# Performance work log

Measured on AMD Instinct MI355X. Metric: run time of the kernel, lower is better.

Reference implementation:

```python
import jax, jax.numpy as jnp
import numpy as np

N, E, F, C, K, H = 100000, 1600000, 64, 32, 8, 36


def setup_inputs() -> dict:
    key = jax.random.key(0)
    ks = jax.random.split(key, 24)
    s = 0.1
    inp = {
        "x": jax.random.normal(ks[0], (N, F), jnp.float32),
        "edge_index": jax.random.randint(ks[1], (2, E), 0, N, dtype=jnp.int32),
        # ChebConv conv1_1: K x [F, H] weights + bias
        "W1_1": jax.random.normal(ks[2], (K, F, H), jnp.float32) * s,
        "b1_1": jnp.zeros((H,), jnp.float32),
        "g1_1": jnp.ones((H,), jnp.float32),
        "be1_1": jnp.zeros((H,), jnp.float32),
        # ChebConv conv1_2: K x [H, H]
        "W1_2": jax.random.normal(ks[3], (K, H, H), jnp.float32) * s,
        "b1_2": jnp.zeros((H,), jnp.float32),
        "g1_2": jnp.ones((H,), jnp.float32),
        "be1_2": jnp.zeros((H,), jnp.float32),
        # GINConv MLP: Linear(F,H) -> ReLU -> Linear(H,H)
        "gin_w1": jax.random.normal(ks[4], (F, H), jnp.float32) * s,
        "gin_b1": jnp.zeros((H,), jnp.float32),
        "gin_w2": jax.random.normal(ks[5], (H, H), jnp.float32) * s,
        "gin_b2": jnp.zeros((H,), jnp.float32),
        "g2": jnp.ones((H,), jnp.float32),
        "be2": jnp.zeros((H,), jnp.float32),
        # conv4: ChebConv K=1 on concat(3H) -> C  (pure linear, no propagation)
        "W4": jax.random.normal(ks[6], (1, 3 * H, C), jnp.float32) * s,
        "b4": jnp.zeros((C,), jnp.float32),
    }
    return inp


def _spmm(w, src, dst, x, n):
    # out[i] = sum_{e: dst_e=i} w_e * x[src_e]
    return jax.ops.segment_sum(w[:, None] * x[src], dst, num_segments=n)


def _cheb(x, src, dst, w, Wk, b):
    # PyG ChebConv with sym norm, lambda_max=2: L_hat = -D^-1/2 A D^-1/2 (loop weight 0)
    n = x.shape[0]
    Kk = Wk.shape[0]
    Tx0 = x
    out = Tx0 @ Wk[0]
    if Kk > 1:
        Tx1 = _spmm(w, src, dst, Tx0, n)
        out = out + Tx1 @ Wk[1]
        for k in range(2, Kk):
            Tx2 = 2.0 * _spmm(w, src, dst, Tx1, n) - Tx0
            out = out + Tx2 @ Wk[k]
            Tx0, Tx1 = Tx1, Tx2
    return out + b


def _bn(x, g, b, eps=1e-5):
    m = jnp.mean(x, axis=0)
    v = jnp.mean(jnp.square(x - m), axis=0)  # biased var, training-mode BN
    return g * (x - m) * jax.lax.rsqrt(v + eps) + b


def reference(x, edge_index, W1_1, b1_1, g1_1, be1_1, W1_2, b1_2, g1_2, be1_2,
              gin_w1, gin_b1, gin_w2, gin_b2, g2, be2, W4, b4):
    src, dst = edge_index[0], edge_index[1]
    n = x.shape[0]
    deg = jax.ops.segment_sum(jnp.ones((src.shape[0],), x.dtype), src, num_segments=n)
    dis = jnp.where(deg > 0, jax.lax.rsqrt(jnp.maximum(deg, 1.0)), 0.0)
    w = -dis[src] * dis[dst]  # scaled Laplacian edge weights

    x1_1 = jax.nn.relu(_bn(_cheb(x, src, dst, w, W1_1, b1_1), g1_1, be1_1))
    x1_2 = jax.nn.relu(_bn(_cheb(x1_1, src, dst, w, W1_2, b1_2), g1_2, be1_2))

    # GINConv (eps=0): nn(x + sum_{j in N(i)} x_j)
    agg = jax.ops.segment_sum(x[src], dst, num_segments=n)
    h = x + agg
    gin = jax.nn.relu(h @ gin_w1 + gin_b1) @ gin_w2 + gin_b2
    x2 = _bn(jax.nn.relu(gin), g2, be2)

    x4 = jnp.concatenate((x1_1, x1_2, x2), axis=1)
    return x4 @ W4[0] + b4
```

## Files before the change

### kernel.cpp

```cpp
#include <hip/hip_runtime.h>

constexpr int N_NODES = 100000;
constexpr int N_EDGES = 1600000;
constexpr int NBK  = 391;
constexpr int NBLK = 640;
constexpr int CHUNK = 2500;
constexpr int LCNT = NBK * NBLK;
constexpr int SCAN_BLKS = (LCNT + 255) / 256;


__device__ __forceinline__ unsigned bf16pack(float a, float b) {
    unsigned ua = __float_as_uint(a), ub = __float_as_uint(b);
    ua += 0x7fffu + ((ua >> 16) & 1u);
    ub += 0x7fffu + ((ub >> 16) & 1u);
    return (ua >> 16) | (ub & 0xffff0000u);
}
__device__ __forceinline__ float bflo(unsigned p) { return __uint_as_float(p << 16); }
__device__ __forceinline__ float bfhi(unsigned p) { return __uint_as_float(p & 0xffff0000u); }


__global__ __launch_bounds__(256) void part_count_kernel(
    const int* __restrict__ ei, int* __restrict__ cntD, int* __restrict__ cntS) {
    __shared__ int hd[NBK], hs[NBK];
    int tid = threadIdx.x;
    for (int i = tid; i < NBK; i += 256) { hd[i] = 0; hs[i] = 0; }
    __syncthreads();
    int e0 = blockIdx.x * CHUNK;
    for (int e = e0 + tid; e < e0 + CHUNK; e += 256) {
        int s = ei[e], d = ei[N_EDGES + e];
        atomicAdd(&hs[s >> 8], 1);
        atomicAdd(&hd[d >> 8], 1);
    }
    __syncthreads();
    for (int i = tid; i < NBK; i += 256) {
        cntD[i * NBLK + blockIdx.x] = hd[i];
        cntS[i * NBLK + blockIdx.x] = hs[i];
    }
}

__global__ __launch_bounds__(256) void scanA_kernel(const int* __restrict__ in,
                                                    int* __restrict__ out,
                                                    int* __restrict__ bsum, int L) {
    __shared__ int sm[256];
    int i = blockIdx.x * 256 + threadIdx.x;
    int v = (i < L) ? in[i] : 0;
    sm[threadIdx.x] = v;
    __syncthreads();
    for (int off = 1; off < 256; off <<= 1) {
        int t = (threadIdx.x >= off) ? sm[threadIdx.x - off] : 0;
        __syncthreads();
        sm[threadIdx.x] += t;
        __syncthreads();
    }
    if (i < L) out[i] = sm[threadIdx.x] - v;
    if (threadIdx.x == 255) bsum[blockIdx.x] = sm[255];
}

__global__ __launch_bounds__(1024) void scanB_kernel(int* __restrict__ bsum, int nb) {
    __shared__ int sm[1024];
    int t = threadIdx.x;
    int v = (t < nb) ? bsum[t] : 0;
    sm[t] = v;
    __syncthreads();
    for (int off = 1; off < 1024; off <<= 1) {
        int u = (t >= off) ? sm[t - off] : 0;
        __syncthreads();
        sm[t] += u;
        __syncthreads();
    }
    if (t < nb) bsum[t] = sm[t] - v;
}

__global__ __launch_bounds__(256) void scanC_kernel(int* __restrict__ out,
                                                    const int* __restrict__ bsum, int L) {
    int i = blockIdx.x * 256 + threadIdx.x;
    if (i < L) out[i] += bsum[blockIdx.x];
}

__global__ __launch_bounds__(256) void part_scatter_kernel(
    const int* __restrict__ ei, const int* __restrict__ scanD,
    const int* __restrict__ scanS, int2* __restrict__ edgepart,
    int* __restrict__ srcpart) {
    __shared__ int curD[NBK], curS[NBK];
    int tid = threadIdx.x;
    for (int i = tid; i < NBK; i += 256) {
        curD[i] = scanD[i * NBLK + blockIdx.x];
        curS[i] = scanS[i * NBLK + blockIdx.x];
    }
    __syncthreads();
    int e0 = blockIdx.x * CHUNK;
    for (int e = e0 + tid; e < e0 + CHUNK; e += 256) {
        int s = ei[e], d = ei[N_EDGES + e];
        int pd = atomicAdd(&curD[d >> 8], 1);
        edgepart[pd] = make_int2(s, d);
        int ps = atomicAdd(&curS[s >> 8], 1);
        srcpart[ps] = s;
    }
}

__global__ __launch_bounds__(256) void deg_kernel(const int* __restrict__ srcpart,
                                                  const int* __restrict__ scanS,
                                                  float* __restrict__ dis) {
    __shared__ int cnt[256];
    int b = blockIdx.x, tid = threadIdx.x;
    cnt[tid] = 0;
    __syncthreads();
    int beg = scanS[b * NBLK];
    int end = (b + 1 < NBK) ? scanS[(b + 1) * NBLK] : N_EDGES;
    for (int j = beg + tid; j < end; j += 256)
        atomicAdd(&cnt[srcpart[j] & 255], 1);
    __syncthreads();
    int node = b * 256 + tid;
    if (node < N_NODES) dis[node] = cnt[tid] > 0 ? rsqrtf((float)cnt[tid]) : 0.f;
}

__global__ __launch_bounds__(256) void csr_kernel(const int2* __restrict__ edgepart,
                                                  const int* __restrict__ scanD,
                                                  const float* __restrict__ dis,
                                                  int* __restrict__ rp,
                                                  int2* __restrict__ csrw) {
    __shared__ int cnt[256];
    __shared__ int lofs[256];
    __shared__ float disl[256];
    int b = blockIdx.x, tid = threadIdx.x;
    int beg = scanD[b * NBLK];
    int end = (b + 1 < NBK) ? scanD[(b + 1) * NBLK] : N_EDGES;
    int node = b * 256 + tid;
    cnt[tid] = 0;
    disl[tid] = (node < N_NODES) ? dis[node] : 0.f;
    __syncthreads();
    for (int j = beg + tid; j < end; j += 256)
        atomicAdd(&cnt[edgepart[j].y & 255], 1);
    __syncthreads();
    int v = cnt[tid];
    lofs[tid] = v;
    __syncthreads();
    for (int off = 1; off < 256; off <<= 1) {
        int t = (tid >= off) ? lofs[tid - off] : 0;
        __syncthreads();
        lofs[tid] += t;
        __syncthreads();
    }
    int myexc = lofs[tid] - v;
    if (node < N_NODES) rp[node] = beg + myexc;
    if (b == NBK - 1 && tid == 0) rp[N_NODES] = N_EDGES;
    __syncthreads();
    lofs[tid] = myexc;
    cnt[tid] = 0;
    __syncthreads();
    for (int j = beg + tid; j < end; j += 256) {
        int2 e = edgepart[j];
        int dl = e.y & 255;
        int pos = beg + lofs[dl] + atomicAdd(&cnt[dl], 1);
        csrw[pos] = make_int2(e.x, __float_as_int(-dis[e.x] * disl[dl]));
    }
}

__global__ void pack_x_kernel(const float* __restrict__ x, uint2* __restrict__ xbf) {
    int i = blockIdx.x * blockDim.x + threadIdx.x;
    if (i >= N_NODES * 16) return;
    float4 v = ((const float4*)x)[i];
    xbf[i] = make_uint2(bf16pack(v.x, v.y), bf16pack(v.z, v.w));
}


template <int FI, int SCALE, bool HAS_B2, bool BN_A, bool FUSE_STATS, bool OUT_BF16>
__global__ __launch_bounds__(256) void cheb_step_kernel(
    const int* __restrict__ rp, const int2* __restrict__ csrw,
    const uint2* __restrict__ INb, const uint2* __restrict__ B2b,
    const float* __restrict__ A, const float* __restrict__ W,
    const float* __restrict__ ss, void* __restrict__ OUT,
    float* __restrict__ partials) {
    __shared__ float Wl[FI * 36];
    __shared__ float Atile[28][FI + 1];
    __shared__ float ls[72];
    int tid = threadIdx.x;
    for (int i = tid; i < FI * 36; i += 252) Wl[i] = W[i];
    int r0 = blockIdx.x * 28;
    for (int i = tid; i < 28 * FI; i += 252) {
        int r = i / FI, f = i % FI;
        int row = r0 + r;
        float v = (row < N_NODES) ? A[row * FI + f] : 0.f;
        if (BN_A) v = fmaxf(fmaf(ss[f], v, ss[36 + f]), 0.f);
        Atile[r][f] = v;
    }
    if (FUSE_STATS && tid < 72) ls[tid] = 0.f;
    __syncthreads();
    int r = tid / 9, c = tid % 9;
    int row = r0 + r;
    bool valid = row < N_NODES;
    float ax = 0, ay = 0, az = 0, aw = 0;
    float bx = 0, by = 0, bz = 0, bw = 0;
    float cx = 0, cy = 0, cz = 0, cw = 0;
    float dx = 0, dy = 0, dz = 0, dw = 0;
    if (SCALE != 0 && valid) {
        int beg = rp[row], end = rp[row + 1];
        int j = beg;
        for (; j + 7 < end; j += 8) {
            int2 e0 = csrw[j],     e1 = csrw[j + 1], e2 = csrw[j + 2], e3 = csrw[j + 3];
            int2 e4 = csrw[j + 4], e5 = csrw[j + 5], e6 = csrw[j + 6], e7 = csrw[j + 7];
            uint2 u0 = INb[e0.x * 16 + c];
            uint2 u1 = INb[e1.x * 16 + c];
            uint2 u2 = INb[e2.x * 16 + c];
            uint2 u3 = INb[e3.x * 16 + c];
            uint2 u4 = INb[e4.x * 16 + c];
            uint2 u5 = INb[e5.x * 16 + c];
            uint2 u6 = INb[e6.x * 16 + c];
            uint2 u7 = INb[e7.x * 16 + c];
            float w0 = __int_as_float(e0.y), w1 = __int_as_float(e1.y);
            float w2 = __int_as_float(e2.y), w3 = __int_as_float(e3.y);
            float w4 = __int_as_float(e4.y), w5 = __int_as_float(e5.y);
            float w6 = __int_as_float(e6.y), w7 = __int_as_float(e7.y);
            ax = fmaf(w0, bflo(u0.x), ax); ay = fmaf(w0, bfhi(u0.x), ay);
            az = fmaf(w0, bflo(u0.y), az); aw = fmaf(w0, bfhi(u0.y), aw);
            bx = fmaf(w1, bflo(u1.x), bx); by = fmaf(w1, bfhi(u1.x), by);
            bz = fmaf(w1, bflo(u1.y), bz); bw = fmaf(w1, bfhi(u1.y), bw);
            cx = fmaf(w2, bflo(u2.x), cx); cy = fmaf(w2, bfhi(u2.x), cy);
            cz = fmaf(w2, bflo(u2.y), cz); cw = fmaf(w2, bfhi(u2.y), cw);
            dx = fmaf(w3, bflo(u3.x), dx); dy = fmaf(w3, bfhi(u3.x), dy);
            dz = fmaf(w3, bflo(u3.y), dz); dw = fmaf(w3, bfhi(u3.y), dw);
            ax = fmaf(w4, bflo(u4.x), ax); ay = fmaf(w4, bfhi(u4.x), ay);
            az = fmaf(w4, bflo(u4.y), az); aw = fmaf(w4, bfhi(u4.y), aw);
            bx = fmaf(w5, bflo(u5.x), bx); by = fmaf(w5, bfhi(u5.x), by);
            bz = fmaf(w5, bflo(u5.y), bz); bw = fmaf(w5, bfhi(u5.y), bw);
            cx = fmaf(w6, bflo(u6.x), cx); cy = fmaf(w6, bfhi(u6.x), cy);
            cz = fmaf(w6, bflo(u6.y), cz); cw = fmaf(w6, bfhi(u6.y), cw);
            dx = fmaf(w7, bflo(u7.x), dx); dy = fmaf(w7, bfhi(u7.x), dy);
            dz = fmaf(w7, bflo(u7.y), dz); dw = fmaf(w7, bfhi(u7.y), dw);
        }
        for (; j + 3 < end; j += 4) {
            int2 e0 = csrw[j], e1 = csrw[j + 1], e2 = csrw[j + 2], e3 = csrw[j + 3];
            uint2 u0 = INb[e0.x * 16 + c];
            uint2 u1 = INb[e1.x * 16 + c];
            uint2 u2 = INb[e2.x * 16 + c];
            uint2 u3 = INb[e3.x * 16 + c];
            float w0 = __int_as_float(e0.y), w1 = __int_as_float(e1.y);
            float w2 = __int_as_float(e2.y), w3 = __int_as_float(e3.y);
            ax = fmaf(w0, bflo(u0.x), ax); ay = fmaf(w0, bfhi(u0.x), ay);
            az = fmaf(w0, bflo(u0.y), az); aw = fmaf(w0, bfhi(u0.y), aw);
            bx = fmaf(w1, bflo(u1.x), bx); by = fmaf(w1, bfhi(u1.x), by);
            bz = fmaf(w1, bflo(u1.y), bz); bw = fmaf(w1, bfhi(u1.y), bw);
            cx = fmaf(w2, bflo(u2.x), cx); cy = fmaf(w2, bfhi(u2.x), cy);
            cz = fmaf(w2, bflo(u2.y), cz); cw = fmaf(w2, bfhi(u2.y), cw);
            dx = fmaf(w3, bflo(u3.x), dx); dy = fmaf(w3, bfhi(u3.x), dy);
            dz = fmaf(w3, bflo(u3.y), dz); dw = fmaf(w3, bfhi(u3.y), dw);
        }
        for (; j < end; ++j) {
            int2 e = csrw[j];
            uint2 u = INb[e.x * 16 + c];
            float w = __int_as_float(e.y);
            ax = fmaf(w, bflo(u.x), ax); ay = fmaf(w, bfhi(u.x), ay);
            az = fmaf(w, bflo(u.y), az); aw = fmaf(w, bfhi(u.y), aw);
        }
        ax += bx + cx + dx; ay += by + cy + dy;
        az += bz + cz + dz; aw += bw + cw + dw;
    }
    float px = 0, py = 0, pz = 0, pw = 0;
    const float4* Wl4 = (const float4*)Wl;
#pragma unroll 4
    for (int f = 0; f < FI; ++f) {
        float a = Atile[r][f];
        float4 wv = Wl4[f * 9 + c];
        px = fmaf(a, wv.x, px); py = fmaf(a, wv.y, py);
        pz = fmaf(a, wv.z, pz); pw = fmaf(a, wv.w, pw);
    }
    const float S = (float)SCALE;
    float4 o;
    o.x = fmaf(S, ax, px); o.y = fmaf(S, ay, py);
    o.z = fmaf(S, az, pz); o.w = fmaf(S, aw, pw);
    if (valid) {
        if (HAS_B2) {
            uint2 u = B2b[row * 16 + c];
            o.x -= bflo(u.x); o.y -= bfhi(u.x);
            o.z -= bflo(u.y); o.w -= bfhi(u.y);
        }
        if (OUT_BF16) {
            ((uint2*)OUT)[row * 16 + c] =
                make_uint2(bf16pack(o.x, o.y), bf16pack(o.z, o.w));
        } else {
            ((float4*)OUT)[row * 9 + c] = o;
        }
        if (FUSE_STATS) {
            atomicAdd(&ls[c * 4 + 0], o.x); atomicAdd(&ls[36 + c * 4 + 0], o.x * o.x);
            atomicAdd(&ls[c * 4 + 1], o.y); atomicAdd(&ls[36 + c * 4 + 1], o.y * o.y);
            atomicAdd(&ls[c * 4 + 2], o.z); atomicAdd(&ls[36 + c * 4 + 2], o.z * o.z);
            atomicAdd(&ls[c * 4 + 3], o.w); atomicAdd(&ls[36 + c * 4 + 3], o.w * o.w);
        }
    }
    if (FUSE_STATS) {
        __syncthreads();
        if (tid < 72) partials[blockIdx.x * 72 + tid] = ls[tid];
    }
}


__global__ __launch_bounds__(256) void gin_fused_kernel(
    const int* __restrict__ rp, const int2* __restrict__ csrw,
    const uint2* __restrict__ Xb,
    const float* __restrict__ w1, const float* __restrict__ b1,
    const float* __restrict__ w2, const float* __restrict__ b2,
    float* __restrict__ OUT, float* __restrict__ partials) {
    __shared__ float W1l[64 * 36];
    __shared__ float W2l[36 * 36];
    __shared__ float B1l[36], B2l[36];
    __shared__ float Ht[16][68];
    __shared__ float M1t[16][40];
    __shared__ float ls[72];
    int tid = threadIdx.x;
    for (int i = tid; i < 64 * 36; i += 256) W1l[i] = w1[i];
    for (int i = tid; i < 36 * 36; i += 256) W2l[i] = w2[i];
    if (tid < 36) { B1l[tid] = b1[tid]; B2l[tid] = b2[tid]; }
    if (tid < 72) ls[tid] = 0.f;
    int r = tid >> 4, l = tid & 15;
    int row = blockIdx.x * 16 + r;
    bool valid = row < N_NODES;
    float hx = 0, hy = 0, hz = 0, hw = 0;
    float gx = 0, gy = 0, gz = 0, gw = 0;
    float px = 0, py = 0, pz = 0, pw = 0;
    float qx = 0, qy = 0, qz = 0, qw = 0;
    if (valid) {
        uint2 us = Xb[row * 16 + l];
        hx = bflo(us.x); hy = bfhi(us.x); hz = bflo(us.y); hw = bfhi(us.y);
        int beg = rp[row], end = rp[row + 1];
        int j = beg;
        for (; j + 7 < end; j += 8) {
            int s0 = csrw[j].x,     s1 = csrw[j + 1].x, s2 = csrw[j + 2].x, s3 = csrw[j + 3].x;
            int s4 = csrw[j + 4].x, s5 = csrw[j + 5].x, s6 = csrw[j + 6].x, s7 = csrw[j + 7].x;
            uint2 u0 = Xb[s0 * 16 + l];
            uint2 u1 = Xb[s1 * 16 + l];
            uint2 u2 = Xb[s2 * 16 + l];
            uint2 u3 = Xb[s3 * 16 + l];
            uint2 u4 = Xb[s4 * 16 + l];
            uint2 u5 = Xb[s5 * 16 + l];
            uint2 u6 = Xb[s6 * 16 + l];
            uint2 u7 = Xb[s7 * 16 + l];
            hx += bflo(u0.x) + bflo(u4.x); hy += bfhi(u0.x) + bfhi(u4.x);
            hz += bflo(u0.y) + bflo(u4.y); hw += bfhi(u0.y) + bfhi(u4.y);
            gx += bflo(u1.x) + bflo(u5.x); gy += bfhi(u1.x) + bfhi(u5.x);
            gz += bflo(u1.y) + bflo(u5.y); gw += bfhi(u1.y) + bfhi(u5.y);
            px += bflo(u2.x) + bflo(u6.x); py += bfhi(u2.x) + bfhi(u6.x);
            pz += bflo(u2.y) + bflo(u6.y); pw += bfhi(u2.y) + bfhi(u6.y);
            qx += bflo(u3.x) + bflo(u7.x); qy += bfhi(u3.x) + bfhi(u7.x);
            qz += bflo(u3.y) + bflo(u7.y); qw += bfhi(u3.y) + bfhi(u7.y);
        }
        for (; j + 3 < end; j += 4) {
            int s0 = csrw[j].x, s1 = csrw[j + 1].x, s2 = csrw[j + 2].x, s3 = csrw[j + 3].x;
            uint2 u0 = Xb[s0 * 16 + l];
            uint2 u1 = Xb[s1 * 16 + l];
            uint2 u2 = Xb[s2 * 16 + l];
            uint2 u3 = Xb[s3 * 16 + l];
            hx += bflo(u0.x); hy += bfhi(u0.x); hz += bflo(u0.y); hw += bfhi(u0.y);
            gx += bflo(u1.x); gy += bfhi(u1.x); gz += bflo(u1.y); gw += bfhi(u1.y);
            px += bflo(u2.x); py += bfhi(u2.x); pz += bflo(u2.y); pw += bfhi(u2.y);
            qx += bflo(u3.x); qy += bfhi(u3.x); qz += bflo(u3.y); qw += bfhi(u3.y);
        }
        for (; j < end; ++j) {
            uint2 u = Xb[csrw[j].x * 16 + l];
            hx += bflo(u.x); hy += bfhi(u.x);
            hz += bflo(u.y); hw += bfhi(u.y);
        }
        hx += gx + px + qx; hy += gy + py + qy;
        hz += gz + pz + qz; hw += gw + pw + qw;
    }
    Ht[r][l * 4 + 0] = hx; Ht[r][l * 4 + 1] = hy;
    Ht[r][l * 4 + 2] = hz; Ht[r][l * 4 + 3] = hw;
    __syncthreads();
    float m1a = B1l[l], m1b = B1l[l + 16], m1c = (l < 4) ? B1l[l + 32] : 0.f;
#pragma unroll 4
    for (int f = 0; f < 64; ++f) {
        float a = Ht[r][f];
        m1a = fmaf(a, W1l[f * 36 + l], m1a);
        m1b = fmaf(a, W1l[f * 36 + l + 16], m1b);
        if (l < 4) m1c = fmaf(a, W1l[f * 36 + l + 32], m1c);
    }
    m1a = fmaxf(m1a, 0.f); m1b = fmaxf(m1b, 0.f); m1c = fmaxf(m1c, 0.f);
    M1t[r][l] = m1a; M1t[r][l + 16] = m1b;
    if (l < 4) M1t[r][l + 32] = m1c;
    __syncthreads();
    float m2a = B2l[l], m2b = B2l[l + 16], m2c = (l < 4) ? B2l[l + 32] : 0.f;
#pragma unroll 4
    for (int f = 0; f < 36; ++f) {
        float a = M1t[r][f];
        m2a = fmaf(a, W2l[f * 36 + l], m2a);
        m2b = fmaf(a, W2l[f * 36 + l + 16], m2b);
        if (l < 4) m2c = fmaf(a, W2l[f * 36 + l + 32], m2c);
    }
    m2a = fmaxf(m2a, 0.f); m2b = fmaxf(m2b, 0.f); m2c = fmaxf(m2c, 0.f);
    if (valid) {
        OUT[row * 36 + l] = m2a;
        OUT[row * 36 + l + 16] = m2b;
        if (l < 4) OUT[row * 36 + l + 32] = m2c;
        atomicAdd(&ls[l], m2a); atomicAdd(&ls[36 + l], m2a * m2a);
        atomicAdd(&ls[l + 16], m2b); atomicAdd(&ls[36 + l + 16], m2b * m2b);
        if (l < 4) { atomicAdd(&ls[l + 32], m2c); atomicAdd(&ls[36 + l + 32], m2c * m2c); }
    }
    __syncthreads();
    if (tid < 72) partials[blockIdx.x * 72 + tid] = ls[tid];
}


__global__ __launch_bounds__(256) void finalize_kernel(
    const float* __restrict__ partials, int nb, const float* __restrict__ g,
    const float* __restrict__ be, float* __restrict__ ss) {
    __shared__ float rs[256], rq[256];
    int c = blockIdx.x;
    int t = threadIdx.x;
    float s = 0.f, q = 0.f;
    for (int i = t; i < nb; i += 256) {
        s += partials[i * 72 + c];
        q += partials[i * 72 + c + 36];
    }
    rs[t] = s; rq[t] = q;
    __syncthreads();
    for (int off = 128; off > 0; off >>= 1) {
        if (t < off) { rs[t] += rs[t + off]; rq[t] += rq[t + off]; }
        __syncthreads();
    }
    if (t == 0) {
        float m = rs[0] / (float)N_NODES;
        float v = rq[0] / (float)N_NODES - m * m;
        float sc = g[c] * rsqrtf(v + 1e-5f);
        ss[c] = sc;
        ss[36 + c] = be[c] - m * sc;
    }
}


__global__ __launch_bounds__(256) void fused3_kernel(
    const float* __restrict__ X1, const float* __restrict__ ssA,
    const float* __restrict__ X2, const float* __restrict__ ssB,
    const float* __restrict__ X3, const float* __restrict__ ssC,
    const float* __restrict__ W, const float* __restrict__ b,
    float* __restrict__ out) {
    __shared__ float Wl[108 * 32];
    __shared__ float Al[64][109];
    int tid = threadIdx.x;
    for (int i = tid; i < 108 * 32; i += 256) Wl[i] = W[i];
    int r0 = blockIdx.x * 64;
    for (int i = tid; i < 64 * 108; i += 256) {
        int r = i / 108, f = i % 108;
        int row = r0 + r;
        float v = 0.f;
        if (row < N_NODES) {
            if (f < 36) {
                v = fmaxf(fmaf(ssA[f], X1[row * 36 + f], ssA[36 + f]), 0.f);
            } else if (f < 72) {
                int ff = f - 36;
                v = fmaxf(fmaf(ssB[ff], X2[row * 36 + ff], ssB[36 + ff]), 0.f);
            } else {
                int ff = f - 72;
                v = fmaf(ssC[ff], X3[row * 36 + ff], ssC[36 + ff]);
            }
        }
        Al[r][f] = v;
    }
    __syncthreads();
    int r = tid >> 2, q = tid & 3;
    int row = r0 + r;
    if (row >= N_NODES) return;
    float acc[8];
#pragma unroll
    for (int j = 0; j < 8; ++j) acc[j] = b[q * 8 + j];
    for (int f = 0; f < 108; ++f) {
        float a = Al[r][f];
#pragma unroll
        for (int j = 0; j < 8; ++j)
            acc[j] = fmaf(a, Wl[f * 32 + q * 8 + j], acc[j]);
    }
#pragma unroll
    for (int j = 0; j < 8; ++j) out[row * 32 + q * 8 + j] = acc[j];
}


extern "C" void kernel_launch(void* const* d_in, const int* in_sizes, int n_in,
                              void* d_out, int out_size, void* d_ws, size_t ws_size,
                              hipStream_t stream) {
    const float* x      = (const float*)d_in[0];
    const int*   ei     = (const int*)d_in[1];
    const float* W1_1   = (const float*)d_in[2];
    const float* g1_1   = (const float*)d_in[4];
    const float* be1_1  = (const float*)d_in[5];
    const float* W1_2   = (const float*)d_in[6];
    const float* g1_2   = (const float*)d_in[8];
    const float* be1_2  = (const float*)d_in[9];
    const float* gin_w1 = (const float*)d_in[10];
    const float* gin_b1 = (const float*)d_in[11];
    const float* gin_w2 = (const float*)d_in[12];
    const float* gin_b2 = (const float*)d_in[13];
    const float* g2     = (const float*)d_in[14];
    const float* be2    = (const float*)d_in[15];
    const float* W4     = (const float*)d_in[16];
    const float* b4     = (const float*)d_in[17];
    float* out = (float*)d_out;

    char* ws = (char*)d_ws;
    size_t off = 0;
    auto alloc = [&](size_t bytes) -> char* {
        char* p = ws + off;
        off = (off + bytes + 255) & ~(size_t)255;
        return p;
    };
    int*   cntD  = (int*)alloc((size_t)LCNT * 4);
    int*   cntS  = (int*)alloc((size_t)LCNT * 4);
    int*   bsum  = (int*)alloc(1024 * 4);
    int*   rp    = (int*)alloc((size_t)(N_NODES + 1) * 4);
    float* dis   = (float*)alloc((size_t)N_NODES * 4);
    int2*  edgepart = (int2*)alloc((size_t)N_EDGES * 8);
    int*   srcpart  = (int*)alloc((size_t)N_EDGES * 4);
    int2*  csrw  = (int2*)alloc((size_t)N_EDGES * 8);
    float* ssA   = (float*)alloc(72 * 4);
    float* ssB   = (float*)alloc(72 * 4);
    float* ssC   = (float*)alloc(72 * 4);
    float* partials = (float*)alloc((size_t)6250 * 72 * 4);
    constexpr size_t NB36 = (size_t)N_NODES * 36 * 4;
    constexpr size_t NBBF = (size_t)N_NODES * 128;
    uint2* xbf = (uint2*)alloc(NBBF);
    uint2* R0  = (uint2*)alloc(NBBF);
    uint2* R1  = (uint2*)alloc(NBBF);
    uint2* R2  = (uint2*)alloc(NBBF);
    float* X1  = (float*)alloc(NB36);
    float* X2  = (float*)alloc(NB36);
    float* X3  = (float*)alloc(NB36);
    if (off > ws_size) return;

    part_count_kernel<<<NBLK, 256, 0, stream>>>(ei, cntD, cntS);
    scanA_kernel<<<SCAN_BLKS, 256, 0, stream>>>(cntD, cntD, bsum, LCNT);
    scanB_kernel<<<1, 1024, 0, stream>>>(bsum, SCAN_BLKS);
    scanC_kernel<<<SCAN_BLKS, 256, 0, stream>>>(cntD, bsum, LCNT);
    scanA_kernel<<<SCAN_BLKS, 256, 0, stream>>>(cntS, cntS, bsum, LCNT);
    scanB_kernel<<<1, 1024, 0, stream>>>(bsum, SCAN_BLKS);
    scanC_kernel<<<SCAN_BLKS, 256, 0, stream>>>(cntS, bsum, LCNT);
    part_scatter_kernel<<<NBLK, 256, 0, stream>>>(ei, cntD, cntS, edgepart, srcpart);
    deg_kernel<<<NBK, 256, 0, stream>>>(srcpart, cntS, dis);
    csr_kernel<<<NBK, 256, 0, stream>>>(edgepart, cntD, dis, rp, csrw);
    pack_x_kernel<<<(N_NODES * 16 + 255) / 256, 256, 0, stream>>>(x, xbf);

    const int STEP_BLKS = (N_NODES + 27) / 28;
    const int GIN_BLKS  = (N_NODES + 15) / 16;
    const int F3_BLKS   = (N_NODES + 63) / 64;

    cheb_step_kernel<64, 0, false, false, false, true><<<STEP_BLKS, 252, 0, stream>>>(
        rp, csrw, nullptr, nullptr, x, W1_1 + 7 * 2304, nullptr, R0, nullptr);
    cheb_step_kernel<64, 2, false, false, false, true><<<STEP_BLKS, 252, 0, stream>>>(
        rp, csrw, R0, nullptr, x, W1_1 + 6 * 2304, nullptr, R1, nullptr);
    cheb_step_kernel<64, 2, true, false, false, true><<<STEP_BLKS, 252, 0, stream>>>(
        rp, csrw, R1, R0, x, W1_1 + 5 * 2304, nullptr, R2, nullptr);
    cheb_step_kernel<64, 2, true, false, false, true><<<STEP_BLKS, 252, 0, stream>>>(
        rp, csrw, R2, R1, x, W1_1 + 4 * 2304, nullptr, R0, nullptr);
    cheb_step_kernel<64, 2, true, false, false, true><<<STEP_BLKS, 252, 0, stream>>>(
        rp, csrw, R0, R2, x, W1_1 + 3 * 2304, nullptr, R1, nullptr);
    cheb_step_kernel<64, 2, true, false, false, true><<<STEP_BLKS, 252, 0, stream>>>(
        rp, csrw, R1, R0, x, W1_1 + 2 * 2304, nullptr, R2, nullptr);
    cheb_step_kernel<64, 2, true, false, false, true><<<STEP_BLKS, 252, 0, stream>>>(
        rp, csrw, R2, R1, x, W1_1 + 1 * 2304, nullptr, R0, nullptr);
    cheb_step_kernel<64, 1, true, false, true, false><<<STEP_BLKS, 252, 0, stream>>>(
        rp, csrw, R0, R2, x, W1_1 + 0 * 2304, nullptr, X1, partials);
    finalize_kernel<<<36, 256, 0, stream>>>(partials, STEP_BLKS, g1_1, be1_1, ssA);

    cheb_step_kernel<36, 0, false, true, false, true><<<STEP_BLKS, 252, 0, stream>>>(
        rp, csrw, nullptr, nullptr, X1, W1_2 + 7 * 1296, ssA, R0, nullptr);
    cheb_step_kernel<36, 2, false, true, false, true><<<STEP_BLKS, 252, 0, stream>>>(
        rp, csrw, R0, nullptr, X1, W1_2 + 6 * 1296, ssA, R1, nullptr);
    cheb_step_kernel<36, 2, true, true, false, true><<<STEP_BLKS, 252, 0, stream>>>(
        rp, csrw, R1, R0, X1, W1_2 + 5 * 1296, ssA, R2, nullptr);
    cheb_step_kernel<36, 2, true, true, false, true><<<STEP_BLKS, 252, 0, stream>>>(
        rp, csrw, R2, R1, X1, W1_2 + 4 * 1296, ssA, R0, nullptr);
    cheb_step_kernel<36, 2, true, true, false, true><<<STEP_BLKS, 252, 0, stream>>>(
        rp, csrw, R0, R2, X1, W1_2 + 3 * 1296, ssA, R1, nullptr);
    cheb_step_kernel<36, 2, true, true, false, true><<<STEP_BLKS, 252, 0, stream>>>(
        rp, csrw, R1, R0, X1, W1_2 + 2 * 1296, ssA, R2, nullptr);
    cheb_step_kernel<36, 2, true, true, false, true><<<STEP_BLKS, 252, 0, stream>>>(
        rp, csrw, R2, R1, X1, W1_2 + 1 * 1296, ssA, R0, nullptr);
    cheb_step_kernel<36, 1, true, true, true, false><<<STEP_BLKS, 252, 0, stream>>>(
        rp, csrw, R0, R2, X1, W1_2 + 0 * 1296, ssA, X2, partials);
    finalize_kernel<<<36, 256, 0, stream>>>(partials, STEP_BLKS, g1_2, be1_2, ssB);

    gin_fused_kernel<<<GIN_BLKS, 256, 0, stream>>>(rp, csrw, xbf, gin_w1, gin_b1,
                                                   gin_w2, gin_b2, X3, partials);
    finalize_kernel<<<36, 256, 0, stream>>>(partials, GIN_BLKS, g2, be2, ssC);

    fused3_kernel<<<F3_BLKS, 256, 0, stream>>>(X1, ssA, X2, ssB, X3, ssC, W4, b4, out);
}
```

Baseline: 989.8 us.

## Project GIN input to hidden width before aggregation and compact bf16 rows

The GIN layer now applies the first linear layer (x @ W1) per node before neighbour aggregation, using linearity, so the gather reads 36-wide bf16 rows instead of 64-wide packed x. The separate x-to-bf16 pack kernel is removed. The bf16 intermediate buffers are compacted from a 16-uint2 row stride to 9, which cuts the bytes moved by every Chebyshev gather step. The risk is that bf16 rounding of the projected features, rather than of x, changes numerics slightly.

```diff
diff --git a/kernel.cpp b/kernel.cpp
--- a/kernel.cpp
+++ b/kernel.cpp
@@ -154,13 +154,6 @@
         int pos = beg + lofs[dl] + atomicAdd(&cnt[dl], 1);
         csrw[pos] = make_int2(e.x, __float_as_int(-dis[e.x] * disl[dl]));
     }
-}
-
-__global__ void pack_x_kernel(const float* __restrict__ x, uint2* __restrict__ xbf) {
-    int i = blockIdx.x * blockDim.x + threadIdx.x;
-    if (i >= N_NODES * 16) return;
-    float4 v = ((const float4*)x)[i];
-    xbf[i] = make_uint2(bf16pack(v.x, v.y), bf16pack(v.z, v.w));
 }
 
 
@@ -199,14 +192,14 @@
         for (; j + 7 < end; j += 8) {
             int2 e0 = csrw[j],     e1 = csrw[j + 1], e2 = csrw[j + 2], e3 = csrw[j + 3];
             int2 e4 = csrw[j + 4], e5 = csrw[j + 5], e6 = csrw[j + 6], e7 = csrw[j + 7];
-            uint2 u0 = INb[e0.x * 16 + c];
-            uint2 u1 = INb[e1.x * 16 + c];
-            uint2 u2 = INb[e2.x * 16 + c];
-            uint2 u3 = INb[e3.x * 16 + c];
-            uint2 u4 = INb[e4.x * 16 + c];
-            uint2 u5 = INb[e5.x * 16 + c];
-            uint2 u6 = INb[e6.x * 16 + c];
-            uint2 u7 = INb[e7.x * 16 + c];
+            uint2 u0 = INb[e0.x * 9 + c];
+            uint2 u1 = INb[e1.x * 9 + c];
+            uint2 u2 = INb[e2.x * 9 + c];
+            uint2 u3 = INb[e3.x * 9 + c];
+            uint2 u4 = INb[e4.x * 9 + c];
+            uint2 u5 = INb[e5.x * 9 + c];
+            uint2 u6 = INb[e6.x * 9 + c];
+            uint2 u7 = INb[e7.x * 9 + c];
             float w0 = __int_as_float(e0.y), w1 = __int_as_float(e1.y);
             float w2 = __int_as_float(e2.y), w3 = __int_as_float(e3.y);
             float w4 = __int_as_float(e4.y), w5 = __int_as_float(e5.y);
@@ -230,10 +223,10 @@
         }
         for (; j + 3 < end; j += 4) {
             int2 e0 = csrw[j], e1 = csrw[j + 1], e2 = csrw[j + 2], e3 = csrw[j + 3];
-            uint2 u0 = INb[e0.x * 16 + c];
-            uint2 u1 = INb[e1.x * 16 + c];
-            uint2 u2 = INb[e2.x * 16 + c];
-            uint2 u3 = INb[e3.x * 16 + c];
+            uint2 u0 = INb[e0.x * 9 + c];
+            uint2 u1 = INb[e1.x * 9 + c];
+            uint2 u2 = INb[e2.x * 9 + c];
+            uint2 u3 = INb[e3.x * 9 + c];
             float w0 = __int_as_float(e0.y), w1 = __int_as_float(e1.y);
             float w2 = __int_as_float(e2.y), w3 = __int_as_float(e3.y);
             ax = fmaf(w0, bflo(u0.x), ax); ay = fmaf(w0, bfhi(u0.x), ay);
@@ -247,7 +240,7 @@
         }
         for (; j < end; ++j) {
             int2 e = csrw[j];
-            uint2 u = INb[e.x * 16 + c];
+            uint2 u = INb[e.x * 9 + c];
             float w = __int_as_float(e.y);
             ax = fmaf(w, bflo(u.x), ax); ay = fmaf(w, bfhi(u.x), ay);
             az = fmaf(w, bflo(u.y), az); aw = fmaf(w, bfhi(u.y), aw);
@@ -270,12 +263,12 @@
     o.z = fmaf(S, az, pz); o.w = fmaf(S, aw, pw);
     if (valid) {
         if (HAS_B2) {
-            uint2 u = B2b[row * 16 + c];
+            uint2 u = B2b[row * 9 + c];
             o.x -= bflo(u.x); o.y -= bfhi(u.x);
             o.z -= bflo(u.y); o.w -= bfhi(u.y);
         }
         if (OUT_BF16) {
-            ((uint2*)OUT)[row * 16 + c] =
+            ((uint2*)OUT)[row * 9 + c] =
                 make_uint2(bf16pack(o.x, o.y), bf16pack(o.z, o.w));
         } else {
             ((float4*)OUT)[row * 9 + c] = o;
@@ -294,105 +287,97 @@
 }
 
 
-__global__ __launch_bounds__(256) void gin_fused_kernel(
+__global__ __launch_bounds__(256) void gin_gather_kernel(
     const int* __restrict__ rp, const int2* __restrict__ csrw,
-    const uint2* __restrict__ Xb,
-    const float* __restrict__ w1, const float* __restrict__ b1,
+    const uint2* __restrict__ Yb, const float* __restrict__ b1,
     const float* __restrict__ w2, const float* __restrict__ b2,
     float* __restrict__ OUT, float* __restrict__ partials) {
-    __shared__ float W1l[64 * 36];
     __shared__ float W2l[36 * 36];
     __shared__ float B1l[36], B2l[36];
-    __shared__ float Ht[16][68];
-    __shared__ float M1t[16][40];
+    __shared__ float M1t[28][37];
     __shared__ float ls[72];
     int tid = threadIdx.x;
-    for (int i = tid; i < 64 * 36; i += 256) W1l[i] = w1[i];
-    for (int i = tid; i < 36 * 36; i += 256) W2l[i] = w2[i];
+    for (int i = tid; i < 36 * 36; i += 252) W2l[i] = w2[i];
     if (tid < 36) { B1l[tid] = b1[tid]; B2l[tid] = b2[tid]; }
     if (tid < 72) ls[tid] = 0.f;
-    int r = tid >> 4, l = tid & 15;
-    int row = blockIdx.x * 16 + r;
+    __syncthreads();
+    int r = tid / 9, c = tid % 9;
+    int row = blockIdx.x * 28 + r;
     bool valid = row < N_NODES;
-    float hx = 0, hy = 0, hz = 0, hw = 0;
-    float gx = 0, gy = 0, gz = 0, gw = 0;
-    float px = 0, py = 0, pz = 0, pw = 0;
-    float qx = 0, qy = 0, qz = 0, qw = 0;
+    float ax = 0, ay = 0, az = 0, aw = 0;
+    float bx = 0, by = 0, bz = 0, bw = 0;
+    float cx = 0, cy = 0, cz = 0, cw = 0;
+    float dx = 0, dy = 0, dz = 0, dw = 0;
     if (valid) {
-        uint2 us = Xb[row * 16 + l];
-        hx = bflo(us.x); hy = bfhi(us.x); hz = bflo(us.y); hw = bfhi(us.y);
+        uint2 us = Yb[row * 9 + c];
+        ax = bflo(us.x); ay = bfhi(us.x); az = bflo(us.y); aw = bfhi(us.y);
         int beg = rp[row], end = rp[row + 1];
         int j = beg;
         for (; j + 7 < end; j += 8) {
             int s0 = csrw[j].x,     s1 = csrw[j + 1].x, s2 = csrw[j + 2].x, s3 = csrw[j + 3].x;
             int s4 = csrw[j + 4].x, s5 = csrw[j + 5].x, s6 = csrw[j + 6].x, s7 = csrw[j + 7].x;
-            uint2 u0 = Xb[s0 * 16 + l];
-            uint2 u1 = Xb[s1 * 16 + l];
-            uint2 u2 = Xb[s2 * 16 + l];
-            uint2 u3 = Xb[s3 * 16 + l];
-            uint2 u4 = Xb[s4 * 16 + l];
-            uint2 u5 = Xb[s5 * 16 + l];
-            uint2 u6 = Xb[s6 * 16 + l];
-            uint2 u7 = Xb[s7 * 16 + l];
-            hx += bflo(u0.x) + bflo(u4.x); hy += bfhi(u0.x) + bfhi(u4.x);
-            hz += bflo(u0.y) + bflo(u4.y); hw += bfhi(u0.y) + bfhi(u4.y);
-            gx += bflo(u1.x) + bflo(u5.x); gy += bfhi(u1.x) + bfhi(u5.x);
-            gz += bflo(u1.y) + bflo(u5.y); gw += bfhi(u1.y) + bfhi(u5.y);
-            px += bflo(u2.x) + bflo(u6.x); py += bfhi(u2.x) + bfhi(u6.x);
-            pz += bflo(u2.y) + bflo(u6.y); pw += bfhi(u2.y) + bfhi(u6.y);
-            qx += bflo(u3.x) + bflo(u7.x); qy += bfhi(u3.x) + bfhi(u7.x);
-            qz += bflo(u3.y) + bflo(u7.y); qw += bfhi(u3.y) + bfhi(u7.y);
+            uint2 u0 = Yb[s0 * 9 + c];
+            uint2 u1 = Yb[s1 * 9 + c];
+            uint2 u2 = Yb[s2 * 9 + c];
+            uint2 u3 = Yb[s3 * 9 + c];
+            uint2 u4 = Yb[s4 * 9 + c];
+            uint2 u5 = Yb[s5 * 9 + c];
+            uint2 u6 = Yb[s6 * 9 + c];
+            uint2 u7 = Yb[s7 * 9 + c];
+            ax += bflo(u0.x) + bflo(u4.x); ay += bfhi(u0.x) + bfhi(u4.x);
+            az += bflo(u0.y) + bflo(u4.y); aw += bfhi(u0.y) + bfhi(u4.y);
+            bx += bflo(u1.x) + bflo(u5.x); by += bfhi(u1.x) + bfhi(u5.x);
+            bz += bflo(u1.y) + bflo(u5.y); bw += bfhi(u1.y) + bfhi(u5.y);
+            cx += bflo(u2.x) + bflo(u6.x); cy += bfhi(u2.x) + bfhi(u6.x);
+            cz += bflo(u2.y) + bflo(u6.y); cw += bfhi(u2.y) + bfhi(u6.y);
+            dx += bflo(u3.x) + bflo(u7.x); dy += bfhi(u3.x) + bfhi(u7.x);
+            dz += bflo(u3.y) + bflo(u7.y); dw += bfhi(u3.y) + bfhi(u7.y);
         }
         for (; j + 3 < end; j += 4) {
             int s0 = csrw[j].x, s1 = csrw[j + 1].x, s2 = csrw[j + 2].x, s3 = csrw[j + 3].x;
-            uint2 u0 = Xb[s0 * 16 + l];
-            uint2 u1 = Xb[s1 * 16 + l];
-            uint2 u2 = Xb[s2 * 16 + l];
-            uint2 u3 = Xb[s3 * 16 + l];
-            hx += bflo(u0.x); hy += bfhi(u0.x); hz += bflo(u0.y); hw += bfhi(u0.y);
-            gx += bflo(u1.x); gy += bfhi(u1.x); gz += bflo(u1.y); gw += bfhi(u1.y);
-            px += bflo(u2.x); py += bfhi(u2.x); pz += bflo(u2.y); pw += bfhi(u2.y);
-            qx += bflo(u3.x); qy += bfhi(u3.x); qz += bflo(u3.y); qw += bfhi(u3.y);
+            uint2 u0 = Yb[s0 * 9 + c];
+            uint2 u1 = Yb[s1 * 9 + c];
+            uint2 u2 = Yb[s2 * 9 + c];
+            uint2 u3 = Yb[s3 * 9 + c];
+            ax += bflo(u0.x); ay += bfhi(u0.x); az += bflo(u0.y); aw += bfhi(u0.y);
+            bx += bflo(u1.x); by += bfhi(u1.x); bz += bflo(u1.y); bw += bfhi(u1.y);
+            cx += bflo(u2.x); cy += bfhi(u2.x); cz += bflo(u2.y); cw += bfhi(u2.y);
+            dx += bflo(u3.x); dy += bfhi(u3.x); dz += bflo(u3.y); dw += bfhi(u3.y);
         }
         for (; j < end; ++j) {
-            uint2 u = Xb[csrw[j].x * 16 + l];
-            hx += bflo(u.x); hy += bfhi(u.x);
-            hz += bflo(u.y); hw += bfhi(u.y);
-        }
-        hx += gx + px + qx; hy += gy + py + qy;
-        hz += gz + pz + qz; hw += gw + pw + qw;
-    }
-    Ht[r][l * 4 + 0] = hx; Ht[r][l * 4 + 1] = hy;
-    Ht[r][l * 4 + 2] = hz; Ht[r][l * 4 + 3] = hw;
-    __syncthreads();
-    float m1a = B1l[l], m1b = B1l[l + 16], m1c = (l < 4) ? B1l[l + 32] : 0.f;
-#pragma unroll 4
-    for (int f = 0; f < 64; ++f) {
-        float a = Ht[r][f];
-        m1a = fmaf(a, W1l[f * 36 + l], m1a);
-        m1b = fmaf(a, W1l[f * 36 + l + 16], m1b);
-        if (l < 4) m1c = fmaf(a, W1l[f * 36 + l + 32], m1c);
-    }
-    m1a = fmaxf(m1a, 0.f); m1b = fmaxf(m1b, 0.f); m1c = fmaxf(m1c, 0.f);
-    M1t[r][l] = m1a; M1t[r][l + 16] = m1b;
-    if (l < 4) M1t[r][l + 32] = m1c;
-    __syncthreads();
-    float m2a = B2l[l], m2b = B2l[l + 16], m2c = (l < 4) ? B2l[l + 32] : 0.f;
+            uint2 u = Yb[csrw[j].x * 9 + c];
+            ax += bflo(u.x); ay += bfhi(u.x);
+            az += bflo(u.y); aw += bfhi(u.y);
+        }
+        ax += bx + cx + dx; ay += by + cy + dy;
+        az += bz + cz + dz; aw += bw + cw + dw;
+    }
+    float m0 = fmaxf(ax + B1l[c * 4 + 0], 0.f);
+    float m1 = fmaxf(ay + B1l[c * 4 + 1], 0.f);
+    float m2 = fmaxf(az + B1l[c * 4 + 2], 0.f);
+    float m3 = fmaxf(aw + B1l[c * 4 + 3], 0.f);
+    M1t[r][c * 4 + 0] = m0; M1t[r][c * 4 + 1] = m1;
+    M1t[r][c * 4 + 2] = m2; M1t[r][c * 4 + 3] = m3;
+    __syncthreads();
+    float o0 = B2l[c * 4 + 0], o1 = B2l[c * 4 + 1];
+    float o2 = B2l[c * 4 + 2], o3 = B2l[c * 4 + 3];
+    const float4* W2l4 = (const float4*)W2l;
 #pragma unroll 4
     for (int f = 0; f < 36; ++f) {
         float a = M1t[r][f];
-        m2a = fmaf(a, W2l[f * 36 + l], m2a);
-        m2b = fmaf(a, W2l[f * 36 + l + 16], m2b);
-        if (l < 4) m2c = fmaf(a, W2l[f * 36 + l + 32], m2c);
-    }
-    m2a = fmaxf(m2a, 0.f); m2b = fmaxf(m2b, 0.f); m2c = fmaxf(m2c, 0.f);
+        float4 wv = W2l4[f * 9 + c];
+        o0 = fmaf(a, wv.x, o0); o1 = fmaf(a, wv.y, o1);
+        o2 = fmaf(a, wv.z, o2); o3 = fmaf(a, wv.w, o3);
+    }
+    o0 = fmaxf(o0, 0.f); o1 = fmaxf(o1, 0.f);
+    o2 = fmaxf(o2, 0.f); o3 = fmaxf(o3, 0.f);
     if (valid) {
-        OUT[row * 36 + l] = m2a;
-        OUT[row * 36 + l + 16] = m2b;
-        if (l < 4) OUT[row * 36 + l + 32] = m2c;
-        atomicAdd(&ls[l], m2a); atomicAdd(&ls[36 + l], m2a * m2a);
-        atomicAdd(&ls[l + 16], m2b); atomicAdd(&ls[36 + l + 16], m2b * m2b);
-        if (l < 4) { atomicAdd(&ls[l + 32], m2c); atomicAdd(&ls[36 + l + 32], m2c * m2c); }
+        float4 o = {o0, o1, o2, o3};
+        ((float4*)OUT)[row * 9 + c] = o;
+        atomicAdd(&ls[c * 4 + 0], o0); atomicAdd(&ls[36 + c * 4 + 0], o0 * o0);
+        atomicAdd(&ls[c * 4 + 1], o1); atomicAdd(&ls[36 + c * 4 + 1], o1 * o1);
+        atomicAdd(&ls[c * 4 + 2], o2); atomicAdd(&ls[36 + c * 4 + 2], o2 * o2);
+        atomicAdd(&ls[c * 4 + 3], o3); atomicAdd(&ls[36 + c * 4 + 3], o3 * o3);
     }
     __syncthreads();
     if (tid < 72) partials[blockIdx.x * 72 + tid] = ls[tid];
@@ -513,8 +498,7 @@
     float* ssC   = (float*)alloc(72 * 4);
     float* partials = (float*)alloc((size_t)6250 * 72 * 4);
     constexpr size_t NB36 = (size_t)N_NODES * 36 * 4;
-    constexpr size_t NBBF = (size_t)N_NODES * 128;
-    uint2* xbf = (uint2*)alloc(NBBF);
+    constexpr size_t NBBF = (size_t)N_NODES * 72;
     uint2* R0  = (uint2*)alloc(NBBF);
     uint2* R1  = (uint2*)alloc(NBBF);
     uint2* R2  = (uint2*)alloc(NBBF);
@@ -533,10 +517,8 @@
     part_scatter_kernel<<<NBLK, 256, 0, stream>>>(ei, cntD, cntS, edgepart, srcpart);
     deg_kernel<<<NBK, 256, 0, stream>>>(srcpart, cntS, dis);
     csr_kernel<<<NBK, 256, 0, stream>>>(edgepart, cntD, dis, rp, csrw);
-    pack_x_kernel<<<(N_NODES * 16 + 255) / 256, 256, 0, stream>>>(x, xbf);
 
     const int STEP_BLKS = (N_NODES + 27) / 28;
-    const int GIN_BLKS  = (N_NODES + 15) / 16;
     const int F3_BLKS   = (N_NODES + 63) / 64;
 
     cheb_step_kernel<64, 0, false, false, false, true><<<STEP_BLKS, 252, 0, stream>>>(
@@ -575,9 +557,11 @@
         rp, csrw, R0, R2, X1, W1_2 + 0 * 1296, ssA, X2, partials);
     finalize_kernel<<<36, 256, 0, stream>>>(partials, STEP_BLKS, g1_2, be1_2, ssB);
 
-    gin_fused_kernel<<<GIN_BLKS, 256, 0, stream>>>(rp, csrw, xbf, gin_w1, gin_b1,
-                                                   gin_w2, gin_b2, X3, partials);
-    finalize_kernel<<<36, 256, 0, stream>>>(partials, GIN_BLKS, g2, be2, ssC);
+    cheb_step_kernel<64, 0, false, false, false, true><<<STEP_BLKS, 252, 0, stream>>>(
+        rp, csrw, nullptr, nullptr, x, gin_w1, nullptr, R0, nullptr);
+    gin_gather_kernel<<<STEP_BLKS, 252, 0, stream>>>(rp, csrw, R0, gin_b1,
+                                                     gin_w2, gin_b2, X3, partials);
+    finalize_kernel<<<36, 256, 0, stream>>>(partials, STEP_BLKS, g2, be2, ssC);
 
     fused3_kernel<<<F3_BLKS, 256, 0, stream>>>(X1, ssA, X2, ssB, X3, ssC, W4, b4, out);
 }
```

After: 970.7 us. No clear change (-1.9%).
